# Kernel tuning notes

Hardware: AMD Instinct MI355X
Metric: run time of the kernel (lower is better)

The kernel has to match this reference:

```python
import jax, jax.numpy as jnp
import numpy as np

N = 100000        # nodes
E = 3200000       # edges (avg degree 32)
D_IN, D_H, D_OUT = 128, 128, 64
EPS = 1e-5        # BatchNorm eps


def setup_inputs() -> dict:
    key = jax.random.key(0)
    ks = jax.random.split(key, 12)
    s = 0.1
    return {
        "x": jax.random.normal(ks[0], (N, D_IN), jnp.float32),
        "edge_index": jax.random.randint(ks[1], (2, E), 0, N, jnp.int32),
        "W1": jax.random.normal(ks[2], (D_IN, D_H), jnp.float32) * s,
        "b1": jnp.zeros((D_H,), jnp.float32),
        "W2": jax.random.normal(ks[3], (D_H, D_H), jnp.float32) * s,
        "b2": jnp.zeros((D_H,), jnp.float32),
        "W3": jax.random.normal(ks[4], (D_H, D_OUT), jnp.float32) * s,
        "b3": jnp.zeros((D_OUT,), jnp.float32),
        "g1": jnp.ones((D_H,), jnp.float32),
        "be1": jnp.zeros((D_H,), jnp.float32),
        "g2": jnp.ones((D_H,), jnp.float32),
        "be2": jnp.zeros((D_H,), jnp.float32),
    }


def reference(x, edge_index, W1, b1, W2, b2, W3, b3, g1, be1, g2, be2):
    # GCNConv normalization: add self-loops, symmetric deg^-1/2 A deg^-1/2
    loop = jnp.arange(N, dtype=edge_index.dtype)
    src = jnp.concatenate([edge_index[0], loop])   # [E+N]
    dst = jnp.concatenate([edge_index[1], loop])   # [E+N]
    deg = jax.ops.segment_sum(jnp.ones(src.shape, x.dtype), dst, num_segments=N)
    dinv = jnp.where(deg > 0, jax.lax.rsqrt(deg), 0.0)
    norm = (dinv[src] * dinv[dst])[:, None]        # [E+N, 1]

    def conv(h, W, b):
        h = h @ W                                   # dense transform [N, d]
        msg = h[src] * norm                         # gather + scale [E+N, d]
        return jax.ops.segment_sum(msg, dst, num_segments=N) + b

    def bn(h, g, be):  # BatchNorm1d over nodes (batch stats, eval-style dropout)
        m = h.mean(axis=0)
        v = h.var(axis=0)
        return (h - m) * jax.lax.rsqrt(v + EPS) * g + be

    h = jax.nn.relu(bn(conv(x, W1, b1), g1, be1))
    h = jax.nn.relu(bn(conv(h, W2, b2), g2, be2))
    h = conv(h, W3, b3)
    return jax.nn.softmax(h, axis=1)
```

## Files before the change

### kernel.cpp

```cpp
#include <hip/hip_runtime.h>
#include <hip/hip_fp16.h>

constexpr int   NN   = 100000;
constexpr int   NE   = 3200000;
constexpr float BN_EPS = 1e-5f;

__global__ __launch_bounds__(256) void k_count(const int* __restrict__ dst,
                                               int* __restrict__ deg,
                                               int* __restrict__ slot) {
  int e = blockIdx.x * 256 + threadIdx.x;
  if (e < NE) slot[e] = atomicAdd(&deg[dst[e]], 1);
}

__global__ __launch_bounds__(256) void k_scan_a(const int* __restrict__ deg,
                                                float* __restrict__ dinv,
                                                int* __restrict__ rowptr,
                                                int* __restrict__ bsum) {
  __shared__ int sd[256];
  int t = threadIdx.x;
  int i = blockIdx.x * 256 + t;
  int v = (i < NN) ? deg[i] : 0;
  if (i < NN) dinv[i] = rsqrtf((float)(v + 1));
  sd[t] = v;
  __syncthreads();
  for (int off = 1; off < 256; off <<= 1) {
    int x = (t >= off) ? sd[t - off] : 0;
    __syncthreads();
    sd[t] += x;
    __syncthreads();
  }
  if (i < NN) rowptr[i] = sd[t] - v;
  if (t == 255) bsum[blockIdx.x] = sd[255];
}

__global__ __launch_bounds__(512) void k_scan_b(int* __restrict__ bsum, int nb) {
  __shared__ int sd[512];
  int t = threadIdx.x;
  int v = (t < nb) ? bsum[t] : 0;
  sd[t] = v;
  __syncthreads();
  for (int off = 1; off < 512; off <<= 1) {
    int x = (t >= off) ? sd[t - off] : 0;
    __syncthreads();
    sd[t] += x;
    __syncthreads();
  }
  if (t < nb) bsum[t] = sd[t] - v;
}

__global__ __launch_bounds__(256) void k_scan_c(int* __restrict__ rowptr,
                                                const int* __restrict__ bsum) {
  int i = blockIdx.x * 256 + threadIdx.x;
  if (i < NN) rowptr[i] += bsum[blockIdx.x];
  if (i == 0) rowptr[NN] = NE;
}

__global__ __launch_bounds__(256) void k_fill(const int* __restrict__ ei,
                                              const int* __restrict__ rowptr,
                                              const int* __restrict__ slot,
                                              int* __restrict__ csrc) {
  int e = blockIdx.x * 256 + threadIdx.x;
  if (e >= NE) return;
  int s = ei[e];
  int d = ei[NE + e];
  csrc[rowptr[d] + slot[e]] = s;
}

template <int BN_, bool FUSE_BN>
__global__ __launch_bounds__(256) void k_gemm(const float* __restrict__ A,
                                              const float* __restrict__ W,
                                              const float* __restrict__ scale,
                                              const float* __restrict__ shift,
                                              const float* __restrict__ dinv,
                                              __half* __restrict__ C) {
  constexpr int NG = BN_ / 64;
  constexpr int AS = 36;
  __shared__ __align__(16) float As[64 * AS];
  __shared__ __align__(16) float Bs[32 * BN_];
  __shared__ __align__(16) float sc[128];
  __shared__ __align__(16) float sh[128];

  const int t = threadIdx.x;
  if (FUSE_BN) {
    if (t < 128) { sc[t] = scale[t]; sh[t] = shift[t]; }
    __syncthreads();
  }

  const int row0 = blockIdx.x * 64;
  const int trow = t >> 4;
  const int tcol = t & 15;

  float acc[4][NG * 4];
#pragma unroll
  for (int i = 0; i < 4; ++i)
#pragma unroll
    for (int j = 0; j < NG * 4; ++j) acc[i][j] = 0.f;

  for (int kt = 0; kt < 4; ++kt) {
#pragma unroll
    for (int i = 0; i < 2; ++i) {
      int fid = t + i * 256;
      int r   = fid >> 3;
      int c4  = fid & 7;
      int row = row0 + r;
      float4 v = make_float4(0.f, 0.f, 0.f, 0.f);
      if (row < NN)
        v = *(const float4*)(A + (size_t)row * 128 + kt * 32 + c4 * 4);
      if (FUSE_BN) {
        int k = kt * 32 + c4 * 4;
        float4 s4 = *(const float4*)&sc[k];
        float4 h4 = *(const float4*)&sh[k];
        v.x = fmaxf(v.x * s4.x + h4.x, 0.f);
        v.y = fmaxf(v.y * s4.y + h4.y, 0.f);
        v.z = fmaxf(v.z * s4.z + h4.z, 0.f);
        v.w = fmaxf(v.w * s4.w + h4.w, 0.f);
      }
      *(float4*)&As[r * AS + c4 * 4] = v;
    }
    constexpr int NB = (32 * BN_) / 4 / 256;
#pragma unroll
    for (int i = 0; i < NB; ++i) {
      int fid = t + i * 256;
      int r   = fid / (BN_ / 4);
      int c4  = fid % (BN_ / 4);
      *(float4*)&Bs[r * BN_ + c4 * 4] =
          *(const float4*)(W + (size_t)(kt * 32 + r) * BN_ + c4 * 4);
    }
    __syncthreads();

#pragma unroll 8
    for (int k = 0; k < 32; ++k) {
      float a0 = As[(4 * trow + 0) * AS + k];
      float a1 = As[(4 * trow + 1) * AS + k];
      float a2 = As[(4 * trow + 2) * AS + k];
      float a3 = As[(4 * trow + 3) * AS + k];
#pragma unroll
      for (int g = 0; g < NG; ++g) {
        float4 b = *(const float4*)&Bs[k * BN_ + g * 64 + tcol * 4];
        acc[0][g*4+0] += a0 * b.x; acc[0][g*4+1] += a0 * b.y;
        acc[0][g*4+2] += a0 * b.z; acc[0][g*4+3] += a0 * b.w;
        acc[1][g*4+0] += a1 * b.x; acc[1][g*4+1] += a1 * b.y;
        acc[1][g*4+2] += a1 * b.z; acc[1][g*4+3] += a1 * b.w;
        acc[2][g*4+0] += a2 * b.x; acc[2][g*4+1] += a2 * b.y;
        acc[2][g*4+2] += a2 * b.z; acc[2][g*4+3] += a2 * b.w;
        acc[3][g*4+0] += a3 * b.x; acc[3][g*4+1] += a3 * b.y;
        acc[3][g*4+2] += a3 * b.z; acc[3][g*4+3] += a3 * b.w;
      }
    }
    __syncthreads();
  }

#pragma unroll
  for (int i = 0; i < 4; ++i) {
    int row = row0 + 4 * trow + i;
    if (row < NN) {
      float dv = dinv[row];
#pragma unroll
      for (int g = 0; g < NG; ++g) {
        union { __half2 h[2]; uint2 u; } pk;
        pk.h[0] = __floats2half2_rn(acc[i][g*4+0] * dv, acc[i][g*4+1] * dv);
        pk.h[1] = __floats2half2_rn(acc[i][g*4+2] * dv, acc[i][g*4+3] * dv);
        *(uint2*)(C + (size_t)row * BN_ + g * 64 + tcol * 4) = pk.u;
      }
    }
  }
}

__global__ __launch_bounds__(256) void k_agg128(const __half* __restrict__ H,
                                                const float* __restrict__ dinv,
                                                const int* __restrict__ rowptr,
                                                const int* __restrict__ srcs,
                                                float* __restrict__ out) {
  int wid  = (blockIdx.x * 256 + threadIdx.x) >> 6;
  int lane = threadIdx.x & 63;
  if (wid >= NN) return;
  const __half2* Hp = (const __half2*)H;
  float2 acc = __half22float2(Hp[(size_t)wid * 64 + lane]);
  int beg = rowptr[wid], end = rowptr[wid + 1];
  int e = beg;
  int end8 = beg + ((end - beg) & ~7);
  for (; e < end8; e += 8) {
    __half2 v0 = Hp[(size_t)srcs[e+0] * 64 + lane];
    __half2 v1 = Hp[(size_t)srcs[e+1] * 64 + lane];
    __half2 v2 = Hp[(size_t)srcs[e+2] * 64 + lane];
    __half2 v3 = Hp[(size_t)srcs[e+3] * 64 + lane];
    __half2 v4 = Hp[(size_t)srcs[e+4] * 64 + lane];
    __half2 v5 = Hp[(size_t)srcs[e+5] * 64 + lane];
    __half2 v6 = Hp[(size_t)srcs[e+6] * 64 + lane];
    __half2 v7 = Hp[(size_t)srcs[e+7] * 64 + lane];
    float2 f0 = __half22float2(v0), f1 = __half22float2(v1);
    float2 f2 = __half22float2(v2), f3 = __half22float2(v3);
    float2 f4 = __half22float2(v4), f5 = __half22float2(v5);
    float2 f6 = __half22float2(v6), f7 = __half22float2(v7);
    acc.x += (f0.x + f1.x) + (f2.x + f3.x) + (f4.x + f5.x) + (f6.x + f7.x);
    acc.y += (f0.y + f1.y) + (f2.y + f3.y) + (f4.y + f5.y) + (f6.y + f7.y);
  }
  for (; e < end; ++e) {
    float2 f = __half22float2(Hp[(size_t)srcs[e] * 64 + lane]);
    acc.x += f.x; acc.y += f.y;
  }
  float di = dinv[wid];
  acc.x *= di; acc.y *= di;
  ((float2*)out)[(size_t)wid * 64 + lane] = acc;
}

__global__ __launch_bounds__(256) void k_agg64_softmax(const __half* __restrict__ H,
                                                       const float* __restrict__ dinv,
                                                       const int* __restrict__ rowptr,
                                                       const int* __restrict__ srcs,
                                                       const float* __restrict__ b3,
                                                       float* __restrict__ out) {
  int wid  = (blockIdx.x * 256 + threadIdx.x) >> 6;
  int lane = threadIdx.x & 63;
  if (wid >= NN) return;
  float acc = __half2float(H[(size_t)wid * 64 + lane]);
  int beg = rowptr[wid], end = rowptr[wid + 1];
  int e = beg;
  int end8 = beg + ((end - beg) & ~7);
  for (; e < end8; e += 8) {
    float v0 = __half2float(H[(size_t)srcs[e+0] * 64 + lane]);
    float v1 = __half2float(H[(size_t)srcs[e+1] * 64 + lane]);
    float v2 = __half2float(H[(size_t)srcs[e+2] * 64 + lane]);
    float v3 = __half2float(H[(size_t)srcs[e+3] * 64 + lane]);
    float v4 = __half2float(H[(size_t)srcs[e+4] * 64 + lane]);
    float v5 = __half2float(H[(size_t)srcs[e+5] * 64 + lane]);
    float v6 = __half2float(H[(size_t)srcs[e+6] * 64 + lane]);
    float v7 = __half2float(H[(size_t)srcs[e+7] * 64 + lane]);
    acc += (v0 + v1) + (v2 + v3) + (v4 + v5) + (v6 + v7);
  }
  for (; e < end; ++e)
    acc += __half2float(H[(size_t)srcs[e] * 64 + lane]);
  acc = acc * dinv[wid] + b3[lane];

  float m = acc;
#pragma unroll
  for (int off = 32; off > 0; off >>= 1) m = fmaxf(m, __shfl_xor(m, off));
  float ev = __expf(acc - m);
  float s = ev;
#pragma unroll
  for (int off = 32; off > 0; off >>= 1) s += __shfl_xor(s, off);
  out[(size_t)wid * 64 + lane] = ev / s;
}

__global__ __launch_bounds__(256) void k_stats(const float* __restrict__ H,
                                               float* __restrict__ S1,
                                               float* __restrict__ S2) {
  int t = threadIdx.x;
  int col  = t & 127;
  int half = t >> 7;
  float s1 = 0.f, s2 = 0.f;
  for (int row = blockIdx.x * 2 + half; row < NN; row += gridDim.x * 2) {
    float v = H[(size_t)row * 128 + col];
    s1 += v; s2 += v * v;
  }
  __shared__ float l1[256], l2[256];
  l1[t] = s1; l2[t] = s2;
  __syncthreads();
  if (t < 128) {
    atomicAdd(&S1[col], l1[t] + l1[t + 128]);
    atomicAdd(&S2[col], l2[t] + l2[t + 128]);
  }
}

__global__ void k_finalize(const float* __restrict__ S1, const float* __restrict__ S2,
                           const float* __restrict__ g,  const float* __restrict__ be,
                           float* __restrict__ scale,    float* __restrict__ shift) {
  int t = threadIdx.x;
  float mean = S1[t] * (1.0f / NN);
  float var  = S2[t] * (1.0f / NN) - mean * mean;
  float is   = rsqrtf(var + BN_EPS);
  float sc   = g[t] * is;
  scale[t] = sc;
  shift[t] = be[t] - mean * sc;
}

extern "C" void kernel_launch(void* const* d_in, const int* in_sizes, int n_in,
                              void* d_out, int out_size, void* d_ws, size_t ws_size,
                              hipStream_t stream) {
  (void)in_sizes; (void)n_in; (void)out_size; (void)ws_size;
  const float* x   = (const float*)d_in[0];
  const int*   ei  = (const int*)d_in[1];
  const float* W1  = (const float*)d_in[2];
  const float* W2  = (const float*)d_in[4];
  const float* W3  = (const float*)d_in[6];
  const float* b3  = (const float*)d_in[7];
  const float* g1  = (const float*)d_in[8];
  const float* be1 = (const float*)d_in[9];
  const float* g2  = (const float*)d_in[10];
  const float* be2 = (const float*)d_in[11];
  float* out = (float*)d_out;

  char* ws = (char*)d_ws;
  size_t off = 0;
  auto take = [&](size_t bytes) -> char* {
    char* p = ws + off;
    off = (off + bytes + 255) & ~(size_t)255;
    return p;
  };
  int*   deg    = (int*)  take((size_t)NN * 4);
  float* S1a    = (float*)take(128 * 4);
  float* S2a    = (float*)take(128 * 4);
  float* S1b    = (float*)take(128 * 4);
  float* S2b    = (float*)take(128 * 4);
  size_t zero_bytes = off;
  float* scale1 = (float*)take(128 * 4);
  float* shift1 = (float*)take(128 * 4);
  float* scale2 = (float*)take(128 * 4);
  float* shift2 = (float*)take(128 * 4);
  float* dinv   = (float*)take((size_t)NN * 4);
  int*   rowptr = (int*)  take((size_t)(NN + 1) * 4);
  int*   bsum   = (int*)  take(1024 * 4);
  int*   slot   = (int*)  take((size_t)NE * 4);
  int*   csrc   = (int*)  take((size_t)NE * 4);
  __half* Hf    = (__half*)take((size_t)NN * 128 * 2);
  float*  bufB  = (float*) take((size_t)NN * 128 * 4);

  (void)hipMemsetAsync(d_ws, 0, zero_bytes, stream);

  const int nbE = (NE + 255) / 256;
  const int nbN = (NN + 255) / 256;
  const int gemmB = (NN + 63) / 64;
  const int aggB  = (NN + 3) / 4;

  k_count <<<nbE, 256, 0, stream>>>(ei + NE, deg, slot);
  k_scan_a<<<nbN, 256, 0, stream>>>(deg, dinv, rowptr, bsum);
  k_scan_b<<<1, 512, 0, stream>>>(bsum, nbN);
  k_scan_c<<<nbN, 256, 0, stream>>>(rowptr, bsum);
  k_fill  <<<nbE, 256, 0, stream>>>(ei, rowptr, slot, csrc);

  k_gemm<128, false><<<gemmB, 256, 0, stream>>>(x, W1, nullptr, nullptr, dinv, Hf);
  k_agg128<<<aggB, 256, 0, stream>>>(Hf, dinv, rowptr, csrc, bufB);
  k_stats<<<1024, 256, 0, stream>>>(bufB, S1a, S2a);
  k_finalize<<<1, 128, 0, stream>>>(S1a, S2a, g1, be1, scale1, shift1);

  k_gemm<128, true><<<gemmB, 256, 0, stream>>>(bufB, W2, scale1, shift1, dinv, Hf);
  k_agg128<<<aggB, 256, 0, stream>>>(Hf, dinv, rowptr, csrc, bufB);
  k_stats<<<1024, 256, 0, stream>>>(bufB, S1b, S2b);
  k_finalize<<<1, 128, 0, stream>>>(S1b, S2b, g2, be2, scale2, shift2);

  k_gemm<64, true><<<gemmB, 256, 0, stream>>>(bufB, W3, scale2, shift2, dinv, Hf);
  k_agg64_softmax<<<aggB, 256, 0, stream>>>(Hf, dinv, rowptr, csrc, b3, out);
}
```

Before: 855.7 us.

## Replace FP32 SIMT GEMM with FP16 MFMA 32x32x16 matrix-core GEMM

Replaces the shared-memory tiled FP32 FMA GEMM with a wave-per-32-rows kernel built on the mfma_f32_32x32x16_f16 builtin. Activations are converted to FP16 in registers, with the BN+ReLU fusion kept, and weights are pre-transposed to FP16 by a small prep kernel. The aim is to offload dense transform FLOPs to matrix cores, at the cost of FP16 input precision. Output stores are now scalar 2-byte writes per lane rather than vectorized, and LDS reuse of weights is dropped in favour of global/L2 loads.

```diff
diff --git a/kernel.cpp b/kernel.cpp
--- a/kernel.cpp
+++ b/kernel.cpp
@@ -4,6 +4,9 @@
 constexpr int   NN   = 100000;
 constexpr int   NE   = 3200000;
 constexpr float BN_EPS = 1e-5f;
+
+typedef _Float16 half8 __attribute__((ext_vector_type(8)));
+typedef float    floatx16 __attribute__((ext_vector_type(16)));
 
 __global__ __launch_bounds__(256) void k_count(const int* __restrict__ dst,
                                                int* __restrict__ deg,
@@ -66,102 +69,72 @@
   csrc[rowptr[d] + slot[e]] = s;
 }
 
+template <int BN_>
+__global__ __launch_bounds__(256) void k_wprep(const float* __restrict__ W,
+                                               _Float16* __restrict__ Wt) {
+  int idx = blockIdx.x * 256 + threadIdx.x;
+  if (idx >= 128 * BN_) return;
+  int k = idx / BN_, n = idx % BN_;
+  Wt[n * 128 + k] = (_Float16)W[idx];
+}
+
 template <int BN_, bool FUSE_BN>
-__global__ __launch_bounds__(256) void k_gemm(const float* __restrict__ A,
-                                              const float* __restrict__ W,
-                                              const float* __restrict__ scale,
-                                              const float* __restrict__ shift,
-                                              const float* __restrict__ dinv,
-                                              __half* __restrict__ C) {
-  constexpr int NG = BN_ / 64;
-  constexpr int AS = 36;
-  __shared__ __align__(16) float As[64 * AS];
-  __shared__ __align__(16) float Bs[32 * BN_];
-  __shared__ __align__(16) float sc[128];
-  __shared__ __align__(16) float sh[128];
-
-  const int t = threadIdx.x;
-  if (FUSE_BN) {
-    if (t < 128) { sc[t] = scale[t]; sh[t] = shift[t]; }
-    __syncthreads();
-  }
-
-  const int row0 = blockIdx.x * 64;
-  const int trow = t >> 4;
-  const int tcol = t & 15;
-
-  float acc[4][NG * 4];
-#pragma unroll
-  for (int i = 0; i < 4; ++i)
-#pragma unroll
-    for (int j = 0; j < NG * 4; ++j) acc[i][j] = 0.f;
-
-  for (int kt = 0; kt < 4; ++kt) {
-#pragma unroll
-    for (int i = 0; i < 2; ++i) {
-      int fid = t + i * 256;
-      int r   = fid >> 3;
-      int c4  = fid & 7;
-      int row = row0 + r;
-      float4 v = make_float4(0.f, 0.f, 0.f, 0.f);
-      if (row < NN)
-        v = *(const float4*)(A + (size_t)row * 128 + kt * 32 + c4 * 4);
-      if (FUSE_BN) {
-        int k = kt * 32 + c4 * 4;
-        float4 s4 = *(const float4*)&sc[k];
-        float4 h4 = *(const float4*)&sh[k];
-        v.x = fmaxf(v.x * s4.x + h4.x, 0.f);
-        v.y = fmaxf(v.y * s4.y + h4.y, 0.f);
-        v.z = fmaxf(v.z * s4.z + h4.z, 0.f);
-        v.w = fmaxf(v.w * s4.w + h4.w, 0.f);
-      }
-      *(float4*)&As[r * AS + c4 * 4] = v;
+__global__ __launch_bounds__(256) void k_mgemm(const float* __restrict__ A,
+                                               const _Float16* __restrict__ Wt,
+                                               const float* __restrict__ scale,
+                                               const float* __restrict__ shift,
+                                               const float* __restrict__ dinv,
+                                               _Float16* __restrict__ C) {
+  constexpr int NCT = BN_ / 32;
+  int wid  = (blockIdx.x * 256 + threadIdx.x) >> 6;
+  int lane = threadIdx.x & 63;
+  if (wid >= NN / 32) return;
+  const int m = lane & 31;
+  const int q = lane >> 5;
+  const int row0 = wid * 32;
+
+  const float* Arow = A + (size_t)(row0 + m) * 128 + q * 8;
+
+  floatx16 acc[NCT] = {};
+
+#pragma unroll
+  for (int s = 0; s < 8; ++s) {
+    float4 a0 = *(const float4*)(Arow + 16 * s);
+    float4 a1 = *(const float4*)(Arow + 16 * s + 4);
+    if (FUSE_BN) {
+      int k0 = 16 * s + q * 8;
+      float4 sc0 = *(const float4*)(scale + k0);
+      float4 sc1 = *(const float4*)(scale + k0 + 4);
+      float4 sh0 = *(const float4*)(shift + k0);
+      float4 sh1 = *(const float4*)(shift + k0 + 4);
+      a0.x = fmaxf(fmaf(a0.x, sc0.x, sh0.x), 0.f);
+      a0.y = fmaxf(fmaf(a0.y, sc0.y, sh0.y), 0.f);
+      a0.z = fmaxf(fmaf(a0.z, sc0.z, sh0.z), 0.f);
+      a0.w = fmaxf(fmaf(a0.w, sc0.w, sh0.w), 0.f);
+      a1.x = fmaxf(fmaf(a1.x, sc1.x, sh1.x), 0.f);
+      a1.y = fmaxf(fmaf(a1.y, sc1.y, sh1.y), 0.f);
+      a1.z = fmaxf(fmaf(a1.z, sc1.z, sh1.z), 0.f);
+      a1.w = fmaxf(fmaf(a1.w, sc1.w, sh1.w), 0.f);
     }
-    constexpr int NB = (32 * BN_) / 4 / 256;
-#pragma unroll
-    for (int i = 0; i < NB; ++i) {
-      int fid = t + i * 256;
-      int r   = fid / (BN_ / 4);
-      int c4  = fid % (BN_ / 4);
-      *(float4*)&Bs[r * BN_ + c4 * 4] =
-          *(const float4*)(W + (size_t)(kt * 32 + r) * BN_ + c4 * 4);
+    half8 af;
+    af[0] = (_Float16)a0.x; af[1] = (_Float16)a0.y;
+    af[2] = (_Float16)a0.z; af[3] = (_Float16)a0.w;
+    af[4] = (_Float16)a1.x; af[5] = (_Float16)a1.y;
+    af[6] = (_Float16)a1.z; af[7] = (_Float16)a1.w;
+#pragma unroll
+    for (int ct = 0; ct < NCT; ++ct) {
+      half8 bf = *(const half8*)(Wt + (size_t)(ct * 32 + m) * 128 + q * 8 + 16 * s);
+      acc[ct] = __builtin_amdgcn_mfma_f32_32x32x16_f16(af, bf, acc[ct], 0, 0, 0);
     }
-    __syncthreads();
-
-#pragma unroll 8
-    for (int k = 0; k < 32; ++k) {
-      float a0 = As[(4 * trow + 0) * AS + k];
-      float a1 = As[(4 * trow + 1) * AS + k];
-      float a2 = As[(4 * trow + 2) * AS + k];
-      float a3 = As[(4 * trow + 3) * AS + k];
-#pragma unroll
-      for (int g = 0; g < NG; ++g) {
-        float4 b = *(const float4*)&Bs[k * BN_ + g * 64 + tcol * 4];
-        acc[0][g*4+0] += a0 * b.x; acc[0][g*4+1] += a0 * b.y;
-        acc[0][g*4+2] += a0 * b.z; acc[0][g*4+3] += a0 * b.w;
-        acc[1][g*4+0] += a1 * b.x; acc[1][g*4+1] += a1 * b.y;
-        acc[1][g*4+2] += a1 * b.z; acc[1][g*4+3] += a1 * b.w;
-        acc[2][g*4+0] += a2 * b.x; acc[2][g*4+1] += a2 * b.y;
-        acc[2][g*4+2] += a2 * b.z; acc[2][g*4+3] += a2 * b.w;
-        acc[3][g*4+0] += a3 * b.x; acc[3][g*4+1] += a3 * b.y;
-        acc[3][g*4+2] += a3 * b.z; acc[3][g*4+3] += a3 * b.w;
-      }
-    }
-    __syncthreads();
-  }
-
-#pragma unroll
-  for (int i = 0; i < 4; ++i) {
-    int row = row0 + 4 * trow + i;
-    if (row < NN) {
-      float dv = dinv[row];
-#pragma unroll
-      for (int g = 0; g < NG; ++g) {
-        union { __half2 h[2]; uint2 u; } pk;
-        pk.h[0] = __floats2half2_rn(acc[i][g*4+0] * dv, acc[i][g*4+1] * dv);
-        pk.h[1] = __floats2half2_rn(acc[i][g*4+2] * dv, acc[i][g*4+3] * dv);
-        *(uint2*)(C + (size_t)row * BN_ + g * 64 + tcol * 4) = pk.u;
-      }
+  }
+
+#pragma unroll
+  for (int ct = 0; ct < NCT; ++ct) {
+#pragma unroll
+    for (int r = 0; r < 16; ++r) {
+      int row = (r & 3) + 8 * (r >> 2) + 4 * q;
+      float dv = dinv[row0 + row];
+      C[(size_t)(row0 + row) * BN_ + ct * 32 + m] = (_Float16)(acc[ct][r] * dv);
     }
   }
 }
@@ -312,14 +285,17 @@
   int*   bsum   = (int*)  take(1024 * 4);
   int*   slot   = (int*)  take((size_t)NE * 4);
   int*   csrc   = (int*)  take((size_t)NE * 4);
-  __half* Hf    = (__half*)take((size_t)NN * 128 * 2);
-  float*  bufB  = (float*) take((size_t)NN * 128 * 4);
+  _Float16* Wt1 = (_Float16*)take((size_t)128 * 128 * 2);
+  _Float16* Wt2 = (_Float16*)take((size_t)128 * 128 * 2);
+  _Float16* Wt3 = (_Float16*)take((size_t)64 * 128 * 2);
+  _Float16* Hf  = (_Float16*)take((size_t)NN * 128 * 2);
+  float*    bufB= (float*)   take((size_t)NN * 128 * 4);
 
   (void)hipMemsetAsync(d_ws, 0, zero_bytes, stream);
 
   const int nbE = (NE + 255) / 256;
   const int nbN = (NN + 255) / 256;
-  const int gemmB = (NN + 63) / 64;
+  const int mgB = (NN / 32 + 3) / 4;
   const int aggB  = (NN + 3) / 4;
 
   k_count <<<nbE, 256, 0, stream>>>(ei + NE, deg, slot);
@@ -328,16 +304,20 @@
   k_scan_c<<<nbN, 256, 0, stream>>>(rowptr, bsum);
   k_fill  <<<nbE, 256, 0, stream>>>(ei, rowptr, slot, csrc);
 
-  k_gemm<128, false><<<gemmB, 256, 0, stream>>>(x, W1, nullptr, nullptr, dinv, Hf);
-  k_agg128<<<aggB, 256, 0, stream>>>(Hf, dinv, rowptr, csrc, bufB);
+  k_wprep<128><<<64, 256, 0, stream>>>(W1, Wt1);
+  k_wprep<128><<<64, 256, 0, stream>>>(W2, Wt2);
+  k_wprep<64> <<<32, 256, 0, stream>>>(W3, Wt3);
+
+  k_mgemm<128, false><<<mgB, 256, 0, stream>>>(x, Wt1, nullptr, nullptr, dinv, Hf);
+  k_agg128<<<aggB, 256, 0, stream>>>((const __half*)Hf, dinv, rowptr, csrc, bufB);
   k_stats<<<1024, 256, 0, stream>>>(bufB, S1a, S2a);
   k_finalize<<<1, 128, 0, stream>>>(S1a, S2a, g1, be1, scale1, shift1);
 
-  k_gemm<128, true><<<gemmB, 256, 0, stream>>>(bufB, W2, scale1, shift1, dinv, Hf);
-  k_agg128<<<aggB, 256, 0, stream>>>(Hf, dinv, rowptr, csrc, bufB);
+  k_mgemm<128, true><<<mgB, 256, 0, stream>>>(bufB, Wt2, scale1, shift1, dinv, Hf);
+  k_agg128<<<aggB, 256, 0, stream>>>((const __half*)Hf, dinv, rowptr, csrc, bufB);
   k_stats<<<1024, 256, 0, stream>>>(bufB, S1b, S2b);
   k_finalize<<<1, 128, 0, stream>>>(S1b, S2b, g2, be2, scale2, shift2);
 
-  k_gemm<64, true><<<gemmB, 256, 0, stream>>>(bufB, W3, scale2, shift2, dinv, Hf);
-  k_agg64_softmax<<<aggB, 256, 0, stream>>>(Hf, dinv, rowptr, csrc, b3, out);
-}
+  k_mgemm<64, true><<<mgB, 256, 0, stream>>>(bufB, Wt3, scale2, shift2, dinv, Hf);
+  k_agg64_softmax<<<aggB, 256, 0, stream>>>((const __half*)Hf, dinv, rowptr, csrc, b3, out);
+}
```

New measurement: 842.4 us. No clear change (-1.5%).
